# Performance work log

Measured on AMD Instinct MI355X. Metric: run time of the kernel, lower is better.

The kernel has to match this reference:

```python
import jax, jax.numpy as jnp
import numpy as np

FACTOR = 5      # ProbAttention sampling factor
NHEAD = 8
LN_EPS = 1e-5


def pos_encoding(L, d):
    pos = np.arange(L, dtype=np.float32)[:, None]
    div = np.exp(np.arange(0, d, 2, dtype=np.float32) * (-np.log(10000.0) / d))
    pe = np.zeros((L, d), np.float32)
    pe[:, 0::2] = np.sin(pos * div)
    pe[:, 1::2] = np.cos(pos * div)
    return jnp.asarray(pe)


def layer_norm(x, s, b):
    mu = x.mean(-1, keepdims=True)
    var = ((x - mu) ** 2).mean(-1, keepdims=True)
    return (x - mu) * jax.lax.rsqrt(var + LN_EPS) * s + b


def prob_attention(x4, key):
    # x4: [B, L, H, D]; self-attention (Q=K=V=x4), mask_flag=False
    B, L, H, D = x4.shape
    q = jnp.transpose(x4, (0, 2, 1, 3))  # [B,H,L,D]
    u = max(1, min(FACTOR * int(np.ceil(np.log(L))), L))  # L_Q == L_K
    # random K-sampling: per-query random subset of keys (shared across B,H)
    idx = jax.random.randint(key, (L, u), 0, L)
    k_s = q[:, :, idx, :]                                # [B,H,L,u,D] irregular gather
    qk_s = jnp.einsum('bhld,bhlsd->bhls', q, k_s)        # [B,H,L,u]
    M = qk_s.max(-1) - qk_s.sum(-1) / L                  # sparsity measure
    _, top = jax.lax.top_k(M, u)                         # [B,H,u] active queries
    q_red = jnp.take_along_axis(q, top[..., None], axis=2)   # [B,H,u,D]
    scale = 1.0 / jnp.sqrt(jnp.float32(D))
    scores = jnp.einsum('bhud,bhkd->bhuk', q_red, q) * scale  # reduced-query scores
    attn = jax.nn.softmax(scores, axis=-1)
    ctx_top = jnp.einsum('bhuk,bhkd->bhud', attn, q)     # V == q here
    # initial context = mean of V (mask_flag=False), scatter top-query results
    ctx = jnp.broadcast_to(q.mean(axis=2, keepdims=True), (B, H, L, D))
    bi = jnp.arange(B)[:, None, None]
    hi = jnp.arange(H)[None, :, None]
    ctx = ctx.at[bi, hi, top].set(ctx_top)
    return jnp.transpose(ctx, (0, 2, 1, 3))  # [B,L,H,D]


def encoder_layer(x4, ln1_s, ln1_b, w1, b1, w2, b2, ln2_s, ln2_b, key):
    B, L, H, D = x4.shape
    new = prob_attention(x4, key)
    x = x4.reshape(B, L, H * D)
    x = layer_norm(x + new.reshape(B, L, H * D), ln1_s, ln1_b)
    # conv1/conv2 with kernel_size=1 == pointwise linears
    y = jax.nn.gelu(jnp.einsum('bld,fd->blf', x, w1) + b1, approximate=False)
    y = jnp.einsum('blf,df->bld', y, w2) + b2
    x = layer_norm(x + y, ln2_s, ln2_b)
    return x.reshape(B, L, H, D)


def distil(x4, factor=2):
    # DistilledAttention: mean-pool over `factor` timesteps (zero-pad to multiple)
    B, L, H, D = x4.shape
    pad = (-L) % factor
    if pad:
        x4 = jnp.pad(x4, ((0, 0), (0, pad), (0, 0), (0, 0)))
    return x4.reshape(B, -1, factor, H, D).mean(axis=2)


def setup_inputs() -> dict:
    key = jax.random.key(0)
    B, L, IN, D, DF, NL = 8, 4096, 64, 512, 2048, 3
    ks = jax.random.split(key, 16)
    s = 0.02
    return {
        'x': jax.random.normal(ks[0], (B, L, IN), jnp.float32),
        'emb_w': jax.random.normal(ks[1], (D, IN), jnp.float32) * s,
        'emb_b': jnp.zeros((D,), jnp.float32),
        'ln1_s': jnp.ones((NL, D), jnp.float32),
        'ln1_b': jnp.zeros((NL, D), jnp.float32),
        'w1': jax.random.normal(ks[2], (NL, DF, D), jnp.float32) * s,
        'b1': jnp.zeros((NL, DF), jnp.float32),
        'w2': jax.random.normal(ks[3], (NL, D, DF), jnp.float32) * s,
        'b2': jnp.zeros((NL, D), jnp.float32),
        'ln2_s': jnp.ones((NL, D), jnp.float32),
        'ln2_b': jnp.zeros((NL, D), jnp.float32),
        'out_w': jax.random.normal(ks[4], (D, D), jnp.float32) * s,
        'out_b': jnp.zeros((D,), jnp.float32),
    }


def reference(x, emb_w, emb_b, ln1_s, ln1_b, w1, b1, w2, b2, ln2_s, ln2_b, out_w, out_b):
    B, L, _ = x.shape
    D = emb_w.shape[0]
    hd = D // NHEAD
    h = jnp.einsum('bli,di->bld', x, emb_w) + emb_b
    h = h + pos_encoding(L, D)[None]
    h = h.reshape(B, L, NHEAD, hd)
    NL = ln1_s.shape[0]
    rkey = jax.random.key(42)  # deterministic ProbSparse sampling
    for i in range(NL):
        h = encoder_layer(h, ln1_s[i], ln1_b[i], w1[i], b1[i], w2[i], b2[i],
                          ln2_s[i], ln2_b[i], jax.random.fold_in(rkey, i))
        if i < NL - 1:
            h = distil(h)
    B2, L2 = h.shape[:2]
    h = h.reshape(B2, L2, D)
    return jnp.einsum('bld,od->blo', h, out_w) + out_b
```

## Files before the change

### kernel.cpp

```cpp
#include <hip/hip_runtime.h>
#include <hip/hip_bf16.h>
#include <math.h>


typedef short short8 __attribute__((ext_vector_type(8)));
typedef float f32x4 __attribute__((ext_vector_type(4)));
typedef unsigned int uint;

__host__ __device__ inline void tf2x32(unsigned k0, unsigned k1,
                                       unsigned x0, unsigned x1,
                                       unsigned& o0, unsigned& o1) {
  unsigned ks2 = k0 ^ k1 ^ 0x1BD11BDAu;
#define TF_R(x, r) x0 += x1; x1 = ((x1 << (r)) | (x1 >> (32 - (r)))); x1 ^= x0;
  x0 += k0; x1 += k1;
  TF_R(x1,13) TF_R(x1,15) TF_R(x1,26) TF_R(x1,6)
  x0 += k1; x1 += ks2 + 1u;
  TF_R(x1,17) TF_R(x1,29) TF_R(x1,16) TF_R(x1,24)
  x0 += ks2; x1 += k0 + 2u;
  TF_R(x1,13) TF_R(x1,15) TF_R(x1,26) TF_R(x1,6)
  x0 += k0; x1 += k1 + 3u;
  TF_R(x1,17) TF_R(x1,29) TF_R(x1,16) TF_R(x1,24)
  x0 += k1; x1 += ks2 + 4u;
  TF_R(x1,13) TF_R(x1,15) TF_R(x1,26) TF_R(x1,6)
  x0 += ks2; x1 += k0 + 5u;
#undef TF_R
  o0 = x0; o1 = x1;
}


__device__ inline unsigned bsplit(float x, float y, float& rx, float& ry) {
  union { __hip_bfloat162 h; unsigned u; } c;
  c.h = __float22bfloat162_rn(make_float2(x, y));
  rx = x - __uint_as_float(c.u << 16);
  ry = y - __uint_as_float(c.u & 0xffff0000u);
  return c.u;
}

__device__ inline void split2u(float4 v0, float4 v1, uint4& H, uint4& M) {
  float r[8]; float d0, d1;
  H.x = bsplit(v0.x, v0.y, r[0], r[1]);
  H.y = bsplit(v0.z, v0.w, r[2], r[3]);
  H.z = bsplit(v1.x, v1.y, r[4], r[5]);
  H.w = bsplit(v1.z, v1.w, r[6], r[7]);
  M.x = bsplit(r[0], r[1], d0, d1);
  M.y = bsplit(r[2], r[3], d0, d1);
  M.z = bsplit(r[4], r[5], d0, d1);
  M.w = bsplit(r[6], r[7], d0, d1);
}

__global__ void k_idx(int* __restrict__ idx, unsigned k2a, unsigned k2b,
                      int n, int mask) {
  int j = blockIdx.x * 256 + threadIdx.x;
  if (j >= n) return;
  unsigned o0, o1;
  tf2x32(k2a, k2b, 0u, (unsigned)j, o0, o1);
  idx[j] = (int)((o0 ^ o1) & (unsigned)mask);
}

__global__ void k_pe(float* __restrict__ pe) {
  int t = blockIdx.x * 256 + threadIdx.x;
  int l = t >> 9, d = t & 511;
  double div = exp((double)(d & ~1) * (-9.210340371976184 / 512.0));
  double ang = (double)l * div;
  pe[t] = (float)((d & 1) ? cos(ang) : sin(ang));
}

__global__ __launch_bounds__(256) void k_embed(const float* __restrict__ x,
    const float* __restrict__ W, const float* __restrict__ eb,
    const float* __restrict__ pe, float* __restrict__ out) {
  __shared__ __align__(16) float xs[16][64];
  int r0 = blockIdx.x * 16;
  int t = threadIdx.x;
  ((float4*)&xs[0][0])[t] = ((const float4*)(x + (size_t)r0 * 64))[t];
  __syncthreads();
  int d0 = t, d1 = t + 256;
  float acc0[16], acc1[16];
#pragma unroll
  for (int r = 0; r < 16; r++) { acc0[r] = 0.f; acc1[r] = 0.f; }
  for (int k = 0; k < 64; k++) {
    float w0 = W[d0 * 64 + k], w1 = W[d1 * 64 + k];
#pragma unroll
    for (int r = 0; r < 16; r++) {
      float xv = xs[r][k];
      acc0[r] = fmaf(xv, w0, acc0[r]);
      acc1[r] = fmaf(xv, w1, acc1[r]);
    }
  }
  float eb0 = eb[d0], eb1 = eb[d1];
#pragma unroll
  for (int r = 0; r < 16; r++) {
    int row = r0 + r;
    int l = row & 4095;
    out[(size_t)row * 512 + d0] = acc0[r] + eb0 + pe[(size_t)l * 512 + d0];
    out[(size_t)row * 512 + d1] = acc1[r] + eb1 + pe[(size_t)l * 512 + d1];
  }
}

__global__ __launch_bounds__(256) void k_colmean1(const float* __restrict__ X,
    double* __restrict__ part, int L, int S) {
  int seg = blockIdx.x, bh = blockIdx.y, b = bh >> 3, h = bh & 7;
  int w = threadIdx.x >> 6, d = threadIdx.x & 63;
  int rows = L / S, r0 = seg * rows;
  const float* base = X + (size_t)b * L * 512 + h * 64 + d;
  double s = 0.0;
  for (int l = r0 + w; l < r0 + rows; l += 4) s += (double)base[(size_t)l * 512];
  __shared__ double red[4][64];
  red[w][d] = s;
  __syncthreads();
  if (w == 0)
    part[((size_t)bh * S + seg) * 64 + d] =
        red[0][d] + red[1][d] + red[2][d] + red[3][d];
}

__global__ void k_colmean2(const double* __restrict__ part,
    float* __restrict__ meanq, int L, int S) {
  int bh = blockIdx.x, d = threadIdx.x;
  const double* p = part + (size_t)bh * S * 64 + d;
  double s = 0.0;
  for (int seg = 0; seg < S; seg++) s += p[seg * 64];
  meanq[bh * 64 + d] = (float)(s / (double)L);
}

__global__ __launch_bounds__(256) void k_M(const float* __restrict__ X,
    const int* __restrict__ idx, float* __restrict__ Mout, int L, int Lsh,
    int u, float invL) {
  int w = threadIdx.x >> 6, lane = threadIdx.x & 63;
  int gl = blockIdx.x * 4 + w;
  int l = gl & (L - 1), bh = gl >> Lsh, b = bh >> 3, h = bh & 7;
  const float* Xbh = X + (size_t)b * L * 512 + h * 64;
  __shared__ float qs[4][64];
  qs[w][lane] = Xbh[(size_t)l * 512 + lane];
  const int s16 = lane >> 2, j = lane & 3;
  float4 qv[4];
#pragma unroll
  for (int c = 0; c < 4; c++) qv[c] = *(const float4*)&qs[w][c * 16 + j * 4];
  const int base = l * u;
  int kx[3];
#pragma unroll
  for (int g = 0; g < 3; g++) {
    int s = g * 16 + s16;
    kx[g] = (s < u) ? idx[base + s] : 0;
  }
  float4 kv[3][4];
#pragma unroll
  for (int g = 0; g < 3; g++) {
    const float* row = Xbh + (size_t)kx[g] * 512 + j * 4;
#pragma unroll
    for (int c = 0; c < 4; c++) kv[g][c] = *(const float4*)(row + c * 16);
  }
  float mv = -1e30f, sv = 0.f;
#pragma unroll
  for (int g = 0; g < 3; g++) {
    float pc[4];
#pragma unroll
    for (int c = 0; c < 4; c++) {
      float p = qv[c].x * kv[g][c].x;
      p = fmaf(qv[c].y, kv[g][c].y, p);
      p = fmaf(qv[c].z, kv[g][c].z, p);
      p = fmaf(qv[c].w, kv[g][c].w, p);
      pc[c] = p;
    }
    float d = (pc[0] + pc[1]) + (pc[2] + pc[3]);
    d += __shfl_xor(d, 1);
    d += __shfl_xor(d, 2);
    if (g * 16 + s16 < u) { mv = fmaxf(mv, d); sv += d; }
  }
  for (int off = 4; off < 64; off <<= 1) {
    mv = fmaxf(mv, __shfl_xor(mv, off));
    sv += __shfl_xor(sv, off);
  }
  if (lane == 0) Mout[(size_t)bh * L + l] = mv - sv * invL;
}

__global__ __launch_bounds__(256) void k_topk(const float* __restrict__ M,
    int* __restrict__ top, int L, int u) {
  __shared__ float mv[4096];
  __shared__ float wv[4];
  __shared__ int wi[4];
  __shared__ int bi_s;
  int bh = blockIdx.x, t = threadIdx.x;
  int w = t >> 6, lane = t & 63;
  const float* Mr = M + (size_t)bh * L;
  for (int k = t; k < L; k += 256) mv[k] = Mr[k];
  __syncthreads();
  float lv = -1e30f; int li = 0x7fffffff;
  for (int k = t; k < L; k += 256) {
    float v = mv[k];
    if (v > lv) { lv = v; li = k; }
  }
  for (int it = 0; it < u; it++) {
    float v = lv; int i = li;
#pragma unroll
    for (int off = 1; off < 64; off <<= 1) {
      float v2 = __shfl_xor(v, off); int i2 = __shfl_xor(i, off);
      if (v2 > v || (v2 == v && i2 < i)) { v = v2; i = i2; }
    }
    if (lane == 0) { wv[w] = v; wi[w] = i; }
    __syncthreads();
    if (t == 0) {
      float bv = wv[0]; int bi = wi[0];
#pragma unroll
      for (int jj = 1; jj < 4; jj++) {
        if (wv[jj] > bv || (wv[jj] == bv && wi[jj] < bi)) { bv = wv[jj]; bi = wi[jj]; }
      }
      top[bh * u + it] = bi;
      mv[bi] = -1e30f;
      bi_s = bi;
    }
    __syncthreads();
    int bi = bi_s;
    if ((bi & 255) == t) {
      lv = -1e30f; li = 0x7fffffff;
      for (int k = t; k < L; k += 256) {
        float v = mv[k];
        if (v > lv) { lv = v; li = k; }
      }
    }
  }
}

__global__ __launch_bounds__(256) void k_scores(const float* __restrict__ X,
    const int* __restrict__ top, float* __restrict__ S, int L, int u) {
  __shared__ __align__(16) float ktT[64][68];
  __shared__ __align__(16) float qred[48][64];
  int bh = blockIdx.y, b = bh >> 3, h = bh & 7;
  int k0 = blockIdx.x * 64;
  int t = threadIdx.x;
  const float* Xbh = X + (size_t)b * L * 512 + h * 64;
#pragma unroll
  for (int it = 0; it < 4; it++) {
    int lin = t + it * 256;
    int kk = lin >> 4, fi = lin & 15;
    float4 v = *(const float4*)(Xbh + (size_t)(k0 + kk) * 512 + fi * 4);
    ktT[fi * 4 + 0][kk] = v.x; ktT[fi * 4 + 1][kk] = v.y;
    ktT[fi * 4 + 2][kk] = v.z; ktT[fi * 4 + 3][kk] = v.w;
  }
#pragma unroll
  for (int it = 0; it < 3; it++) {
    int lin = t + it * 256;
    int ur = lin >> 4, fi = lin & 15;
    if (ur < u) {
      int row = top[bh * u + ur];
      *(float4*)(&qred[ur][fi * 4]) = *(const float4*)(Xbh + (size_t)row * 512 + fi * 4);
    } else if (ur < 48) {
      *(float4*)(&qred[ur][fi * 4]) = make_float4(0.f, 0.f, 0.f, 0.f);
    }
  }
  __syncthreads();
  int xq = t & 15, y = t >> 4;
  float acc[3][4];
#pragma unroll
  for (int j = 0; j < 3; j++)
#pragma unroll
    for (int e = 0; e < 4; e++) acc[j][e] = 0.f;
  for (int d = 0; d < 64; d++) {
    float4 kv = *(const float4*)(&ktT[d][xq * 4]);
#pragma unroll
    for (int j = 0; j < 3; j++) {
      float qv = qred[y * 3 + j][d];
      acc[j][0] = fmaf(qv, kv.x, acc[j][0]);
      acc[j][1] = fmaf(qv, kv.y, acc[j][1]);
      acc[j][2] = fmaf(qv, kv.z, acc[j][2]);
      acc[j][3] = fmaf(qv, kv.w, acc[j][3]);
    }
  }
#pragma unroll
  for (int j = 0; j < 3; j++) {
    int ur = y * 3 + j;
    if (ur < u) {
      float4 o = make_float4(acc[j][0] * 0.125f, acc[j][1] * 0.125f,
                             acc[j][2] * 0.125f, acc[j][3] * 0.125f);
      *(float4*)(S + ((size_t)(bh * u + ur)) * L + k0 + xq * 4) = o;
    }
  }
}

__global__ __launch_bounds__(256) void k_smstat(const float* __restrict__ S,
    float* __restrict__ MX, double* __restrict__ INV, int L, int u) {
  int ur = blockIdx.x, bh = blockIdx.y;
  const float* Srow = S + ((size_t)(bh * u + ur)) * L;
  int t = threadIdx.x;
  __shared__ float rm[256];
  __shared__ double rs[256];
  float m = -1e30f;
  for (int k = t; k < L; k += 256) m = fmaxf(m, Srow[k]);
  rm[t] = m; __syncthreads();
  for (int off = 128; off; off >>= 1) {
    if (t < off) rm[t] = fmaxf(rm[t], rm[t + off]);
    __syncthreads();
  }
  float mx = rm[0];
  double s = 0.0;
  for (int k = t; k < L; k += 256) s += (double)expf(Srow[k] - mx);
  rs[t] = s; __syncthreads();
  for (int off = 128; off; off >>= 1) {
    if (t < off) rs[t] += rs[t + off];
    __syncthreads();
  }
  if (t == 0) { MX[bh * 48 + ur] = mx; INV[bh * 48 + ur] = 1.0 / rs[0]; }
}

#define PVSEG 8
__global__ __launch_bounds__(256) void k_pv(const float* __restrict__ X,
    const float* __restrict__ S, const float* __restrict__ MX,
    float* __restrict__ P2, int L, int u) {
  __shared__ __align__(16) float xs[32][64];
  __shared__ __align__(16) float wsm[32][52];
  int seg = blockIdx.x, bh = blockIdx.y, b = bh >> 3, h = bh & 7;
  int t = threadIdx.x, w = t >> 6, lane = t & 63;
  int rows = L / PVSEG, l0 = seg * rows;
  const float* Xb = X + (size_t)b * L * 512 + h * 64;
  int li = lane & 31, par = lane >> 5;
  const float* Sp[6]; float mxl[6]; int val[6];
#pragma unroll
  for (int jj = 0; jj < 6; jj++) {
    int ur = w * 12 + par + jj * 2;
    val[jj] = (ur < u);
    Sp[jj] = S + (size_t)(bh * u + (val[jj] ? ur : 0)) * L + l0 + li;
    mxl[jj] = val[jj] ? MX[bh * 48 + ur] : 0.f;
  }
  float acc[12];
#pragma unroll
  for (int j = 0; j < 12; j++) acc[j] = 0.f;
  int xr = t >> 4, xf = t & 15;
  for (int c = 0; c < rows; c += 32) {
    __syncthreads();
    *(float4*)&xs[xr][xf * 4] =
        *(const float4*)(Xb + (size_t)(l0 + c + xr) * 512 + xf * 4);
    *(float4*)&xs[16 + xr][xf * 4] =
        *(const float4*)(Xb + (size_t)(l0 + c + 16 + xr) * 512 + xf * 4);
#pragma unroll
    for (int jj = 0; jj < 6; jj++) {
      float e = val[jj] ? expf(Sp[jj][c] - mxl[jj]) : 0.f;
      wsm[li][w * 12 + par + jj * 2] = e;
    }
    __syncthreads();
#pragma unroll 2
    for (int l = 0; l < 32; l++) {
      float xv = xs[l][lane];
      float4 w0 = *(const float4*)&wsm[l][w * 12];
      float4 w1 = *(const float4*)&wsm[l][w * 12 + 4];
      float4 w2 = *(const float4*)&wsm[l][w * 12 + 8];
      acc[0]  = fmaf(w0.x, xv, acc[0]);  acc[1]  = fmaf(w0.y, xv, acc[1]);
      acc[2]  = fmaf(w0.z, xv, acc[2]);  acc[3]  = fmaf(w0.w, xv, acc[3]);
      acc[4]  = fmaf(w1.x, xv, acc[4]);  acc[5]  = fmaf(w1.y, xv, acc[5]);
      acc[6]  = fmaf(w1.z, xv, acc[6]);  acc[7]  = fmaf(w1.w, xv, acc[7]);
      acc[8]  = fmaf(w2.x, xv, acc[8]);  acc[9]  = fmaf(w2.y, xv, acc[9]);
      acc[10] = fmaf(w2.z, xv, acc[10]); acc[11] = fmaf(w2.w, xv, acc[11]);
    }
  }
  float* P = P2 + ((size_t)(bh * PVSEG + seg) * 48 + w * 12) * 64 + lane;
#pragma unroll
  for (int j = 0; j < 12; j++) P[j * 64] = acc[j];
}

__global__ __launch_bounds__(256) void k_pvred(const float* __restrict__ P2,
    const double* __restrict__ INV, const int* __restrict__ top,
    float* __restrict__ CTX, char* __restrict__ FLG, int L, int u) {
  int bh = blockIdx.x;
  const float* Pb = P2 + (size_t)bh * PVSEG * 48 * 64;
  for (int e = threadIdx.x; e < u * 64; e += 256) {
    int ur = e >> 6, d = e & 63;
    const float* p = Pb + ur * 64 + d;
    const int st = 48 * 64;
    double s = ((double)p[0] + (double)p[st]) +
               ((double)p[2 * st] + (double)p[3 * st]) +
               ((double)p[4 * st] + (double)p[5 * st]) +
               ((double)p[6 * st] + (double)p[7 * st]);
    double tot = s * INV[bh * 48 + ur];
    CTX[((size_t)bh * 48 + ur) * 64 + d] = (float)tot;
    if (d == 0) FLG[(size_t)bh * L + top[bh * u + ur]] = (char)(ur + 1);
  }
}

__global__ __launch_bounds__(256) void k_ln1(float* __restrict__ X,
    const char* __restrict__ FLG, const float* __restrict__ CTX,
    const float* __restrict__ meanq, const float* __restrict__ gs,
    const float* __restrict__ gb, char* __restrict__ XPbase, int L, int Lsh) {
  int w = threadIdx.x >> 6, lane = threadIdx.x & 63;
  int row = blockIdx.x * 4 + w;
  int b = row >> Lsh, l = row & (L - 1);
  float* xr = X + (size_t)row * 512;
  int h = lane >> 3;
  int bh = b * 8 + h;
  int flag = (int)FLG[(size_t)bh * L + l];
  float4 c0, c1;
  if (flag) {
    const float* cx = CTX + ((size_t)bh * 48 + (flag - 1)) * 64 + (lane & 7) * 8;
    c0 = *(const float4*)cx; c1 = *(const float4*)(cx + 4);
  } else {
    const float* mq = meanq + b * 512 + lane * 8;
    c0 = *(const float4*)mq; c1 = *(const float4*)(mq + 4);
  }
  float4 x0 = *(const float4*)(xr + lane * 8);
  float4 x1 = *(const float4*)(xr + lane * 8 + 4);
  float v[8] = { x0.x + c0.x, x0.y + c0.y, x0.z + c0.z, x0.w + c0.w,
                 x1.x + c1.x, x1.y + c1.y, x1.z + c1.z, x1.w + c1.w };
  double s = 0.0, s2 = 0.0;
#pragma unroll
  for (int i = 0; i < 8; i++) { s += (double)v[i]; s2 += (double)v[i] * (double)v[i]; }
  for (int off = 32; off; off >>= 1) { s += __shfl_xor(s, off); s2 += __shfl_xor(s2, off); }
  double mu = s * (1.0 / 512.0);
  double var = s2 * (1.0 / 512.0) - mu * mu;
  float rsd = (float)(1.0 / sqrt(var + 1e-5));
  float muf = (float)mu;
  float4 g0 = *(const float4*)(gs + lane * 8);
  float4 g1 = *(const float4*)(gs + lane * 8 + 4);
  float4 b0 = *(const float4*)(gb + lane * 8);
  float4 b1 = *(const float4*)(gb + lane * 8 + 4);
  float4 y0 = make_float4((v[0] - muf) * rsd * g0.x + b0.x,
                          (v[1] - muf) * rsd * g0.y + b0.y,
                          (v[2] - muf) * rsd * g0.z + b0.z,
                          (v[3] - muf) * rsd * g0.w + b0.w);
  float4 y1 = make_float4((v[4] - muf) * rsd * g1.x + b1.x,
                          (v[5] - muf) * rsd * g1.y + b1.y,
                          (v[6] - muf) * rsd * g1.z + b1.z,
                          (v[7] - muf) * rsd * g1.w + b1.w);
  *(float4*)(xr + lane * 8) = y0;
  *(float4*)(xr + lane * 8 + 4) = y1;
  int c = row >> 13, ml = row & 8191;
  char* P = XPbase + ((size_t)c << 24);
  const size_t psz = (size_t)8192 * 512 * 2;
  int k = lane * 8;
  size_t off = ((size_t)(ml >> 4) * 16 + (k >> 5)) * 1024
             + (size_t)(((k >> 3) & 3) * 256 + (ml & 15) * 16);
  uint4 H, Md;
  split2u(y0, y1, H, Md);
  *(uint4*)(P + off) = H;
  *(uint4*)(P + psz + off) = Md;
}

__global__ __launch_bounds__(256) void k_ln2(const float* __restrict__ X,
    const float* __restrict__ Y2, const float* __restrict__ gs,
    const float* __restrict__ gb, float* __restrict__ out) {
  int w = threadIdx.x >> 6, lane = threadIdx.x & 63;
  int orow = blockIdx.x * 4 + w;
  float o[8] = {0.f,0.f,0.f,0.f,0.f,0.f,0.f,0.f};
  for (int p = 0; p < 2; p++) {
    int row = orow * 2 + p;
    const float* xr = X + (size_t)row * 512;
    const float* yr = Y2 + (size_t)row * 512;
    float v[8]; double s = 0.0, s2 = 0.0;
#pragma unroll
    for (int i = 0; i < 8; i++) {
      float val = xr[lane + i * 64] + yr[lane + i * 64];
      v[i] = val; s += (double)val; s2 += (double)val * (double)val;
    }
    for (int off = 32; off; off >>= 1) { s += __shfl_xor(s, off); s2 += __shfl_xor(s2, off); }
    double mu = s * (1.0 / 512.0);
    double var = s2 * (1.0 / 512.0) - mu * mu;
    float rsd = (float)(1.0 / sqrt(var + 1e-5));
    float muf = (float)mu;
#pragma unroll
    for (int i = 0; i < 8; i++)
      o[i] += (v[i] - muf) * rsd * gs[lane + i * 64] + gb[lane + i * 64];
  }
#pragma unroll
  for (int i = 0; i < 8; i++)
    out[(size_t)orow * 512 + lane + i * 64] = o[i] * 0.5f;
}

__global__ __launch_bounds__(256) void k_ln2p(const float* __restrict__ X,
    const float* __restrict__ Y2, const float* __restrict__ gs,
    const float* __restrict__ gb, char* __restrict__ P) {
  int w = threadIdx.x >> 6, lane = threadIdx.x & 63;
  int row = blockIdx.x * 4 + w;
  const float* xr = X + (size_t)row * 512;
  const float* yr = Y2 + (size_t)row * 512;
  float4 x0 = *(const float4*)(xr + lane * 8);
  float4 x1 = *(const float4*)(xr + lane * 8 + 4);
  float4 z0 = *(const float4*)(yr + lane * 8);
  float4 z1 = *(const float4*)(yr + lane * 8 + 4);
  float v[8] = { x0.x + z0.x, x0.y + z0.y, x0.z + z0.z, x0.w + z0.w,
                 x1.x + z1.x, x1.y + z1.y, x1.z + z1.z, x1.w + z1.w };
  double s = 0.0, s2 = 0.0;
#pragma unroll
  for (int i = 0; i < 8; i++) { s += (double)v[i]; s2 += (double)v[i] * (double)v[i]; }
  for (int off = 32; off; off >>= 1) { s += __shfl_xor(s, off); s2 += __shfl_xor(s2, off); }
  double mu = s * (1.0 / 512.0);
  double var = s2 * (1.0 / 512.0) - mu * mu;
  float rsd = (float)(1.0 / sqrt(var + 1e-5));
  float muf = (float)mu;
  float4 g0 = *(const float4*)(gs + lane * 8);
  float4 g1 = *(const float4*)(gs + lane * 8 + 4);
  float4 b0 = *(const float4*)(gb + lane * 8);
  float4 b1 = *(const float4*)(gb + lane * 8 + 4);
  float4 y0 = make_float4((v[0] - muf) * rsd * g0.x + b0.x,
                          (v[1] - muf) * rsd * g0.y + b0.y,
                          (v[2] - muf) * rsd * g0.z + b0.z,
                          (v[3] - muf) * rsd * g0.w + b0.w);
  float4 y1 = make_float4((v[4] - muf) * rsd * g1.x + b1.x,
                          (v[5] - muf) * rsd * g1.y + b1.y,
                          (v[6] - muf) * rsd * g1.z + b1.z,
                          (v[7] - muf) * rsd * g1.w + b1.w);
  const size_t psz = (size_t)8192 * 512 * 2;
  int k = lane * 8;
  size_t off = ((size_t)(row >> 4) * 16 + (k >> 5)) * 1024
             + (size_t)(((k >> 3) & 3) * 256 + (row & 15) * 16);
  uint4 H, Md;
  split2u(y0, y1, H, Md);
  *(uint4*)(P + off) = H;
  *(uint4*)(P + psz + off) = Md;
}

__global__ void k_splitX(const float* __restrict__ X, char* __restrict__ P,
                         int K, int total8) {
  int f = blockIdx.x * 256 + threadIdx.x;
  if (f >= total8) return;
  int k8 = f % (K >> 3), m = f / (K >> 3);
  int k = k8 * 8;
  const float* src = X + (size_t)m * K + k;
  float4 v0 = *(const float4*)(src);
  float4 v1 = *(const float4*)(src + 4);
  uint4 H, Md;
  split2u(v0, v1, H, Md);
  size_t psz = (size_t)total8 * 16;
  size_t off = ((size_t)(m >> 4) * (K >> 5) + (k >> 5)) * 1024
             + (size_t)(((k >> 3) & 3) * 256 + (m & 15) * 16);
  *(uint4*)(P + off) = H;
  *(uint4*)(P + psz + off) = Md;
}

__device__ __forceinline__ void async16(void* lds, const void* g) {
  __builtin_amdgcn_global_load_lds(
      (const __attribute__((address_space(1))) uint*)g,
      (__attribute__((address_space(3))) uint*)lds, 16, 0, 0);
}

template <int MT, int GELU, int PLANES_OUT>
__global__ __launch_bounds__(256) void k_gemm6(const char* __restrict__ AP,
    const char* __restrict__ BP, const float* __restrict__ bias,
    void* __restrict__ Cout, int N, int K) {
  __shared__ __align__(16) char lds[(MT * 2 + 16) * 1024];
  const int t = threadIdx.x;
  const int w = t >> 6, lane = t & 63;
  const int bx = blockIdx.x, by = blockIdx.y;
  const int quad = lane >> 4, rit = lane & 15;
  const int Mrows = gridDim.y * (MT * 16);
  const size_t psA = (size_t)Mrows * K * 2;
  const size_t psB = (size_t)N * K * 2;
  const int KB = K >> 5;
  char* ldsA = lds;
  char* ldsB = lds + MT * 2 * 1024;
  const int wm = (w >> 1) * (MT / 2), wn = (w & 1) * 4;
  f32x4 acc[MT / 2][4];
#pragma unroll
  for (int i = 0; i < MT / 2; i++)
#pragma unroll
    for (int j = 0; j < 4; j++) acc[i][j] = (f32x4){0.f, 0.f, 0.f, 0.f};
  for (int kt = 0; kt < KB; kt++) {
#pragma unroll
    for (int r = 0; r < MT / 2; r++) {
      int q = w + 4 * r;
      int p = q / MT, tt = q % MT;
      async16(ldsA + (p * MT + tt) * 1024,
              AP + p * psA + ((size_t)(by * MT + tt) * KB + kt) * 1024 + lane * 16);
    }
#pragma unroll
    for (int r = 0; r < 4; r++) {
      int q = w + 4 * r;
      int p = q >> 3, tt = q & 7;
      async16(ldsB + (p * 8 + tt) * 1024,
              BP + p * psB + ((size_t)(bx * 8 + tt) * KB + kt) * 1024 + lane * 16);
    }
    __syncthreads();
    short8 af[2][MT / 2];
#pragma unroll
    for (int p = 0; p < 2; p++)
#pragma unroll
      for (int mi = 0; mi < MT / 2; mi++)
        af[p][mi] = *(const short8*)(ldsA + (p * MT + wm + mi) * 1024 + lane * 16);
#pragma unroll
    for (int ni = 0; ni < 4; ni++) {
      const char* bb = ldsB + (wn + ni) * 1024 + lane * 16;
      short8 bh = *(const short8*)(bb);
      short8 bm = *(const short8*)(bb + 8192);
#pragma unroll
      for (int mi = 0; mi < MT / 2; mi++) {
        f32x4 c = acc[mi][ni];
        c = __builtin_amdgcn_mfma_f32_16x16x32_bf16(af[0][mi], bh, c, 0, 0, 0);
        c = __builtin_amdgcn_mfma_f32_16x16x32_bf16(af[0][mi], bm, c, 0, 0, 0);
        c = __builtin_amdgcn_mfma_f32_16x16x32_bf16(af[1][mi], bh, c, 0, 0, 0);
        acc[mi][ni] = c;
      }
    }
    __syncthreads();
  }
  const int n0 = bx * 128, m_base = by * (MT * 16);
  if (!PLANES_OUT) {
    float* C = (float*)Cout;
#pragma unroll
    for (int mi = 0; mi < MT / 2; mi++) {
      const int gr0 = m_base + (wm + mi) * 16 + quad * 4;
#pragma unroll
      for (int ni = 0; ni < 4; ni++) {
        const int gc = n0 + (wn + ni) * 16 + rit;
        const float bia = bias[gc];
#pragma unroll
        for (int e = 0; e < 4; e++) {
          float v = acc[mi][ni][e] + bia;
          if (GELU) v = 0.5f * v * (1.0f + erff(v * 0.7071067811865476f));
          C[(size_t)(gr0 + e) * N + gc] = v;
        }
      }
    }
  } else {
    char* CP = (char*)Cout;
    const size_t psC = (size_t)Mrows * N * 2;
    float* lf = (float*)lds;
    for (int h = 0; h < 2; h++) {
      __syncthreads();
      if ((w & 1) == h) {
#pragma unroll
        for (int ni = 0; ni < 4; ni++) {
          const float bia = bias[n0 + h * 64 + ni * 16 + rit];
#pragma unroll
          for (int mi = 0; mi < MT / 2; mi++) {
            const int ml0 = (wm + mi) * 16 + quad * 4;
#pragma unroll
            for (int e = 0; e < 4; e++) {
              float v = acc[mi][ni][e] + bia;
              if (GELU) v = 0.5f * v * (1.0f + erff(v * 0.7071067811865476f));
              lf[(ml0 + e) * 64 + ni * 16 + rit] = v;
            }
          }
        }
      }
      __syncthreads();
#pragma unroll
      for (int it = 0; it < (MT * 16 * 8) / 256; it++) {
        int p = it * 256 + t;
        int ml = p >> 3, n8 = p & 7;
        float4 v0 = *(const float4*)&lf[ml * 64 + n8 * 8];
        float4 v1 = *(const float4*)&lf[ml * 64 + n8 * 8 + 4];
        uint4 H, Md;
        split2u(v0, v1, H, Md);
        int mg = m_base + ml, kg = n0 + h * 64 + n8 * 8;
        size_t off = ((size_t)(mg >> 4) * (N >> 5) + (kg >> 5)) * 1024
                   + (size_t)(((kg >> 3) & 3) * 256 + (mg & 15) * 16);
        *(uint4*)(CP + off) = H;
        *(uint4*)(CP + psC + off) = Md;
      }
    }
  }
}

extern "C" void kernel_launch(void* const* d_in, const int* in_sizes, int n_in,
                              void* d_out, int out_size, void* d_ws, size_t ws_size,
                              hipStream_t stream) {
  const float* x     = (const float*)d_in[0];
  const float* emb_w = (const float*)d_in[1];
  const float* emb_b = (const float*)d_in[2];
  const float* ln1_s = (const float*)d_in[3];
  const float* ln1_b = (const float*)d_in[4];
  const float* w1    = (const float*)d_in[5];
  const float* b1    = (const float*)d_in[6];
  const float* w2    = (const float*)d_in[7];
  const float* b2    = (const float*)d_in[8];
  const float* ln2_s = (const float*)d_in[9];
  const float* ln2_b = (const float*)d_in[10];
  const float* out_w = (const float*)d_in[11];
  const float* out_b = (const float*)d_in[12];
  float* outp = (float*)d_out;

  char* ws = (char*)d_ws;
  if (ws_size < (212ULL << 20)) return;
  float* PE    = (float*)(ws);
  char*  W1S   = ws;
  float* BUF[3] = { (float*)(ws + (8ULL << 20)),
                    (float*)(ws + (72ULL << 20)),
                    (float*)(ws + (136ULL << 20)) };
  char*  W2S   = ws + (200ULL << 20);
  float* MB    = (float*)(ws + (206ULL << 20));
  int*   IDX   = (int*)  (ws + (207ULL << 20));
  int*   TOP   = (int*)  (ws + (208ULL << 20));
  float* MEANQ = (float*)(ws + (208ULL << 20) + (64 << 10));
  float* MXB   = (float*)(ws + (208ULL << 20) + (128 << 10));
  double* INVB = (double*)(ws + (208ULL << 20) + (192 << 10));
  double* PART = (double*)(ws + (209ULL << 20));
  char*  FLG   = ws + (210ULL << 20);
  float* CTX   = (float*)(ws + (210ULL << 20) + (512 << 10));

  k_pe<<<4096 * 512 / 256, 256, 0, stream>>>(PE);
  k_embed<<<(8 * 4096) / 16, 256, 0, stream>>>(x, emb_w, emb_b, PE, BUF[0]);

  const int Ls[3] = {4096, 2048, 1024};
  const int Lshs[3] = {12, 11, 10};
  const int us[3] = {45, 40, 35};
  int xi = 0, ai = 1, yi = 2;
  char* FINALP = nullptr;
  for (int layer = 0; layer < 3; layer++) {
    const int L = Ls[layer], u = us[layer];
    float* X = BUF[xi]; float* A = BUF[ai]; float* Y = BUF[yi];

    k_splitX<<<(2048 * 512 / 8) / 256, 256, 0, stream>>>(
        w1 + (size_t)layer * 2048 * 512, W1S, 512, 2048 * 512 / 8);
    k_splitX<<<(512 * 2048 / 8) / 256, 256, 0, stream>>>(
        w2 + (size_t)layer * 512 * 2048, W2S, 2048, 512 * 2048 / 8);

    unsigned Ka, Kb, k2a, k2b;
    tf2x32(0u, 42u, 0u, (unsigned)layer, Ka, Kb);
    tf2x32(Ka, Kb, 0u, 1u, k2a, k2b);
    const int n = L * u;
    k_idx<<<(n + 255) / 256, 256, 0, stream>>>(IDX, k2a, k2b, n, L - 1);
    const int S = 32;
    k_colmean1<<<dim3(S, 64), 256, 0, stream>>>(X, PART, L, S);
    k_colmean2<<<64, 64, 0, stream>>>(PART, MEANQ, L, S);
    k_M<<<64 * L / 4, 256, 0, stream>>>(X, IDX, MB, L, Lshs[layer], u,
                                        1.0f / (float)L);
    k_topk<<<64, 256, 0, stream>>>(MB, TOP, L, u);
    hipMemsetAsync(FLG, 0, (size_t)64 * L, stream);
    k_scores<<<dim3(L / 64, 64), 256, 0, stream>>>(X, TOP, Y, L, u);
    float* P2 = (float*)((char*)Y + (48ULL << 20));
    k_smstat<<<dim3(u, 64), 256, 0, stream>>>(Y, MXB, INVB, L, u);
    k_pv<<<dim3(PVSEG, 64), 256, 0, stream>>>(X, Y, MXB, P2, L, u);
    k_pvred<<<64, 256, 0, stream>>>(P2, INVB, TOP, CTX, FLG, L, u);
    k_ln1<<<8 * L / 4, 256, 0, stream>>>(X, FLG, CTX, MEANQ,
                                         ln1_s + layer * 512,
                                         ln1_b + layer * 512, (char*)A,
                                         L, Lshs[layer]);

    char* YP = (char*)Y;
    const int chunks = (8 * L) / 8192;
    for (int c = 0; c < chunks; c++) {
      float* Ac = A + (size_t)c * 8192 * 512;
      char* XP = (char*)Ac;
      k_gemm6<8, 1, 1><<<dim3(16, 64), 256, 0, stream>>>(
          XP, W1S, b1 + layer * 2048, YP, 2048, 512);
      k_gemm6<4, 0, 0><<<dim3(4, 128), 256, 0, stream>>>(
          YP, W2S, b2 + layer * 512, Ac, 512, 2048);
    }
    if (layer < 2) {
      k_ln2<<<8 * (L / 2) / 4, 256, 0, stream>>>(X, A, ln2_s + layer * 512,
                                                 ln2_b + layer * 512, Y);
    } else {
      FINALP = (char*)Y;
      k_ln2p<<<8 * L / 4, 256, 0, stream>>>(X, A, ln2_s + layer * 512,
                                            ln2_b + layer * 512, FINALP);
    }
    int tswap = xi; xi = yi; yi = ai; ai = tswap;
  }
  char* WOS = W2S;
  k_splitX<<<(512 * 512 / 8) / 256, 256, 0, stream>>>(out_w, WOS, 512, 512 * 512 / 8);
  k_gemm6<4, 0, 0><<<dim3(4, 128), 256, 0, stream>>>(
      FINALP, WOS, out_b, outp, 512, 512);
}
```

Before: 2.182 ms.

## Fuse softmax statistics into PV kernel with split-softmax merge; swizzle GEMM block order

```diff
diff --git a/kernel.cpp b/kernel.cpp
--- a/kernel.cpp
+++ b/kernel.cpp
@@ -130,6 +130,7 @@
   const float* Xbh = X + (size_t)b * L * 512 + h * 64;
   __shared__ float qs[4][64];
   qs[w][lane] = Xbh[(size_t)l * 512 + lane];
+  __syncthreads();
   const int s16 = lane >> 2, j = lane & 3;
   float4 qv[4];
 #pragma unroll
@@ -275,35 +276,10 @@
   }
 }
 
-__global__ __launch_bounds__(256) void k_smstat(const float* __restrict__ S,
-    float* __restrict__ MX, double* __restrict__ INV, int L, int u) {
-  int ur = blockIdx.x, bh = blockIdx.y;
-  const float* Srow = S + ((size_t)(bh * u + ur)) * L;
-  int t = threadIdx.x;
-  __shared__ float rm[256];
-  __shared__ double rs[256];
-  float m = -1e30f;
-  for (int k = t; k < L; k += 256) m = fmaxf(m, Srow[k]);
-  rm[t] = m; __syncthreads();
-  for (int off = 128; off; off >>= 1) {
-    if (t < off) rm[t] = fmaxf(rm[t], rm[t + off]);
-    __syncthreads();
-  }
-  float mx = rm[0];
-  double s = 0.0;
-  for (int k = t; k < L; k += 256) s += (double)expf(Srow[k] - mx);
-  rs[t] = s; __syncthreads();
-  for (int off = 128; off; off >>= 1) {
-    if (t < off) rs[t] += rs[t + off];
-    __syncthreads();
-  }
-  if (t == 0) { MX[bh * 48 + ur] = mx; INV[bh * 48 + ur] = 1.0 / rs[0]; }
-}
-
 #define PVSEG 8
 __global__ __launch_bounds__(256) void k_pv(const float* __restrict__ X,
-    const float* __restrict__ S, const float* __restrict__ MX,
-    float* __restrict__ P2, int L, int u) {
+    const float* __restrict__ S, float* __restrict__ P2,
+    float* __restrict__ MS, float* __restrict__ SS, int L, int u) {
   __shared__ __align__(16) float xs[32][64];
   __shared__ __align__(16) float wsm[32][52];
   int seg = blockIdx.x, bh = blockIdx.y, b = bh >> 3, h = bh & 7;
@@ -311,17 +287,31 @@
   int rows = L / PVSEG, l0 = seg * rows;
   const float* Xb = X + (size_t)b * L * 512 + h * 64;
   int li = lane & 31, par = lane >> 5;
-  const float* Sp[6]; float mxl[6]; int val[6];
+  const float* Sp[6]; int val[6];
 #pragma unroll
   for (int jj = 0; jj < 6; jj++) {
     int ur = w * 12 + par + jj * 2;
     val[jj] = (ur < u);
     Sp[jj] = S + (size_t)(bh * u + (val[jj] ? ur : 0)) * L + l0 + li;
-    mxl[jj] = val[jj] ? MX[bh * 48 + ur] : 0.f;
-  }
-  float acc[12];
+  }
+  float mloc[6];
+#pragma unroll
+  for (int jj = 0; jj < 6; jj++) mloc[jj] = -1e30f;
+  for (int c = 0; c < rows; c += 32) {
+#pragma unroll
+    for (int jj = 0; jj < 6; jj++) mloc[jj] = fmaxf(mloc[jj], Sp[jj][c]);
+  }
+#pragma unroll
+  for (int jj = 0; jj < 6; jj++) {
+#pragma unroll
+    for (int off = 1; off < 32; off <<= 1)
+      mloc[jj] = fmaxf(mloc[jj], __shfl_xor(mloc[jj], off));
+  }
+  float acc[12], esum[6];
 #pragma unroll
   for (int j = 0; j < 12; j++) acc[j] = 0.f;
+#pragma unroll
+  for (int j = 0; j < 6; j++) esum[j] = 0.f;
   int xr = t >> 4, xf = t & 15;
   for (int c = 0; c < rows; c += 32) {
     __syncthreads();
@@ -331,7 +321,8 @@
         *(const float4*)(Xb + (size_t)(l0 + c + 16 + xr) * 512 + xf * 4);
 #pragma unroll
     for (int jj = 0; jj < 6; jj++) {
-      float e = val[jj] ? expf(Sp[jj][c] - mxl[jj]) : 0.f;
+      float e = val[jj] ? expf(Sp[jj][c] - mloc[jj]) : 0.f;
+      esum[jj] += e;
       wsm[li][w * 12 + par + jj * 2] = e;
     }
     __syncthreads();
@@ -352,22 +343,53 @@
   float* P = P2 + ((size_t)(bh * PVSEG + seg) * 48 + w * 12) * 64 + lane;
 #pragma unroll
   for (int j = 0; j < 12; j++) P[j * 64] = acc[j];
+#pragma unroll
+  for (int jj = 0; jj < 6; jj++) {
+    float es = esum[jj];
+#pragma unroll
+    for (int off = 1; off < 32; off <<= 1) es += __shfl_xor(es, off);
+    if (li == 0) {
+      int ur = w * 12 + par + jj * 2;
+      MS[((size_t)bh * PVSEG + seg) * 48 + ur] = mloc[jj];
+      SS[((size_t)bh * PVSEG + seg) * 48 + ur] = es;
+    }
+  }
 }
 
 __global__ __launch_bounds__(256) void k_pvred(const float* __restrict__ P2,
-    const double* __restrict__ INV, const int* __restrict__ top,
-    float* __restrict__ CTX, char* __restrict__ FLG, int L, int u) {
+    const float* __restrict__ MS, const float* __restrict__ SS,
+    const int* __restrict__ top, float* __restrict__ CTX,
+    char* __restrict__ FLG, int L, int u) {
   int bh = blockIdx.x;
+  int t = threadIdx.x;
   const float* Pb = P2 + (size_t)bh * PVSEG * 48 * 64;
-  for (int e = threadIdx.x; e < u * 64; e += 256) {
+  const float* Mb = MS + (size_t)bh * PVSEG * 48;
+  const float* Sb = SS + (size_t)bh * PVSEG * 48;
+  __shared__ float fac[PVSEG][48];
+  __shared__ double dens[48];
+  if (t < u) {
+    float mx = Mb[t];
+#pragma unroll
+    for (int s = 1; s < PVSEG; s++) mx = fmaxf(mx, Mb[s * 48 + t]);
+    double den = 0.0;
+#pragma unroll
+    for (int s = 0; s < PVSEG; s++) {
+      float f = expf(Mb[s * 48 + t] - mx);
+      fac[s][t] = f;
+      den += (double)Sb[s * 48 + t] * (double)f;
+    }
+    dens[t] = den;
+  }
+  __syncthreads();
+  for (int e = t; e < u * 64; e += 256) {
     int ur = e >> 6, d = e & 63;
     const float* p = Pb + ur * 64 + d;
     const int st = 48 * 64;
-    double s = ((double)p[0] + (double)p[st]) +
-               ((double)p[2 * st] + (double)p[3 * st]) +
-               ((double)p[4 * st] + (double)p[5 * st]) +
-               ((double)p[6 * st] + (double)p[7 * st]);
-    double tot = s * INV[bh * 48 + ur];
+    double num = 0.0;
+#pragma unroll
+    for (int s = 0; s < PVSEG; s++)
+      num += (double)p[s * st] * (double)fac[s][ur];
+    double tot = num / dens[ur];
     CTX[((size_t)bh * 48 + ur) * 64 + d] = (float)tot;
     if (d == 0) FLG[(size_t)bh * L + top[bh * u + ur]] = (char)(ur + 1);
   }
@@ -534,7 +556,11 @@
   __shared__ __align__(16) char lds[(MT * 2 + 16) * 1024];
   const int t = threadIdx.x;
   const int w = t >> 6, lane = t & 63;
-  const int bx = blockIdx.x, by = blockIdx.y;
+  int lin = blockIdx.y * gridDim.x + blockIdx.x;
+  const int nb = gridDim.x * gridDim.y;
+  lin = (lin & 7) * (nb >> 3) + (lin >> 3);
+  const int shx = 31 - __clz(gridDim.x);
+  const int bx = lin & (gridDim.x - 1), by = lin >> shx;
   const int quad = lane >> 4, rit = lane & 15;
   const int Mrows = gridDim.y * (MT * 16);
   const size_t psA = (size_t)Mrows * K * 2;
@@ -675,8 +701,6 @@
   int*   IDX   = (int*)  (ws + (207ULL << 20));
   int*   TOP   = (int*)  (ws + (208ULL << 20));
   float* MEANQ = (float*)(ws + (208ULL << 20) + (64 << 10));
-  float* MXB   = (float*)(ws + (208ULL << 20) + (128 << 10));
-  double* INVB = (double*)(ws + (208ULL << 20) + (192 << 10));
   double* PART = (double*)(ws + (209ULL << 20));
   char*  FLG   = ws + (210ULL << 20);
   float* CTX   = (float*)(ws + (210ULL << 20) + (512 << 10));
@@ -712,9 +736,10 @@
     hipMemsetAsync(FLG, 0, (size_t)64 * L, stream);
     k_scores<<<dim3(L / 64, 64), 256, 0, stream>>>(X, TOP, Y, L, u);
     float* P2 = (float*)((char*)Y + (48ULL << 20));
-    k_smstat<<<dim3(u, 64), 256, 0, stream>>>(Y, MXB, INVB, L, u);
-    k_pv<<<dim3(PVSEG, 64), 256, 0, stream>>>(X, Y, MXB, P2, L, u);
-    k_pvred<<<64, 256, 0, stream>>>(P2, INVB, TOP, CTX, FLG, L, u);
+    float* MS = (float*)((char*)Y + (56ULL << 20));
+    float* SS = (float*)((char*)Y + (57ULL << 20));
+    k_pv<<<dim3(PVSEG, 64), 256, 0, stream>>>(X, Y, P2, MS, SS, L, u);
+    k_pvred<<<64, 256, 0, stream>>>(P2, MS, SS, TOP, CTX, FLG, L, u);
     k_ln1<<<8 * L / 4, 256, 0, stream>>>(X, FLG, CTX, MEANQ,
                                          ln1_s + layer * 512,
                                          ln1_b + layer * 512, (char*)A,
```

Result: faster. 2.095 ms (-4.0%).
